# Optimization experiments

Hardware: AMD Instinct MI355X
Metric: run time of the kernel (lower is better)

## Reference

```python
import jax, jax.numpy as jnp
import numpy as np

B, C, H, W = 4, 384, 64, 64
NH = 8
HD = C // NH
SR = 2
SCALE = HD ** -0.5
Hs, Ws = H // SR, W // SR
NK = Hs * Ws


def setup_inputs() -> dict:
    key = jax.random.key(0)
    ks = jax.random.split(key, 8)
    s = 0.02
    return {
        "x": jax.random.normal(ks[0], (B, C, H, W), jnp.float32),
        "Wq": jax.random.normal(ks[1], (C, C), jnp.float32) * s,
        "Wk": jax.random.normal(ks[2], (C, C), jnp.float32) * s,
        "Wv": jax.random.normal(ks[3], (C, C), jnp.float32) * s,
        "Wsr": jax.random.normal(ks[4], (C, C, SR, SR), jnp.float32) * s,
        "bsr": jnp.zeros((C,), jnp.float32),
        "Wp": jax.random.normal(ks[5], (C, C), jnp.float32) * s,
        "bp": jnp.zeros((C,), jnp.float32),
        "rel_h": jax.random.normal(ks[6], (1, NH, HD, 1, Hs), jnp.float32),
        "rel_w": jax.random.normal(ks[7], (1, NH, HD, Ws, 1), jnp.float32),
    }


def _mhsa(x, Wq, Wk, Wv, Wsr, bsr, Wp, bp, rel_h, rel_w):
    Bq = x.shape[0]
    # 1x1 conv == channel matmul
    q = jnp.einsum('oc,bchw->bohw', Wq, x).reshape(Bq, NH, HD, H * W)
    # spatial reduction: Conv2d(kernel=SR, stride=SR); norm defaults to Identity
    xsr = jax.lax.conv_general_dilated(
        x, Wsr, window_strides=(SR, SR), padding='VALID',
        dimension_numbers=('NCHW', 'OIHW', 'NCHW')) + bsr[None, :, None, None]
    k = jnp.einsum('oc,bchw->bohw', Wk, xsr).reshape(Bq, NH, HD, NK)
    v = jnp.einsum('oc,bchw->bohw', Wv, xsr).reshape(Bq, NH, HD, NK)
    # relative positional bias fused into keys
    pos = (rel_h + rel_w).reshape(1, NH, HD, NK)
    k = (k + pos) * SCALE
    # attn[b,h,n,m] = q^T k, softmax over keys (dropout is identity at p=0)
    attn = jax.nn.softmax(jnp.einsum('bhdn,bhdm->bhnm', q, k), axis=-1)
    out = jnp.einsum('bhdm,bhnm->bhdn', v, attn).reshape(Bq, C, H, W)
    out = jnp.einsum('oc,bchw->bohw', Wp, out) + bp[None, :, None, None]
    return out


def reference(x, Wq, Wk, Wv, Wsr, bsr, Wp, bp, rel_h, rel_w):
    return _mhsa(x, Wq, Wk, Wv, Wsr, bsr, Wp, bp, rel_h, rel_w)
```

## Files before the change

### kernel.cpp

```cpp
#include <hip/hip_runtime.h>
#include <hip/hip_bf16.h>
#include <math.h>

typedef __attribute__((ext_vector_type(8))) short b16x8;
typedef __attribute__((ext_vector_type(4))) short b16x4;
typedef __attribute__((ext_vector_type(4))) float floatx4;
typedef __attribute__((ext_vector_type(16))) float f32x16;

constexpr int BATCH = 4, CCH = 384, NQ = 4096, NHD = 8, HDIM = 48, NK = 1024;
constexpr float SCALE = 0.14433756729740643f;
constexpr float SCALE_L2E = 0.14433756729740643f * 1.4426950408889634f;

__device__ inline unsigned short f2bf(float f) {
    unsigned u = __builtin_bit_cast(unsigned, f);
    u += 0x7fffu + ((u >> 16) & 1u);
    return (unsigned short)(u >> 16);
}

__device__ __forceinline__ void g2lds16(const void* g, void* l) {
    __builtin_amdgcn_global_load_lds(
        (const __attribute__((address_space(1))) unsigned int*)g,
        (__attribute__((address_space(3))) unsigned int*)l, 16, 0, 0);
}

__global__ void cvt_all(const float* __restrict__ Wq, const float* __restrict__ Wk,
                        const float* __restrict__ Wv, const float* __restrict__ Wsr,
                        const float* __restrict__ Wp,
                        short* __restrict__ WqB, short* __restrict__ WkvB,
                        short* __restrict__ WsrB, short* __restrict__ WpB) {
    int job = blockIdx.y;
    if (job == 3) {
        for (int i = blockIdx.x * 256 + threadIdx.x; i < 589824; i += gridDim.x * 256) {
            int o = i / 1536, r = i - o * 1536;
            WsrB[o * 1536 + (r & 3) * 384 + (r >> 2)] = (short)f2bf(Wsr[i]);
        }
        return;
    }
    const float* src; short* dst;
    if (job == 0)      { src = Wq;  dst = WqB; }
    else if (job == 1) { src = Wk;  dst = WkvB; }
    else if (job == 2) { src = Wv;  dst = WkvB + 147456; }
    else               { src = Wp;  dst = WpB; }
    for (int i = blockIdx.x * 256 + threadIdx.x; i < 147456; i += gridDim.x * 256)
        dst[i] = (short)f2bf(src[i]);
}

__global__ void t1_kern(const float* __restrict__ x, short* __restrict__ xT) {
    int b = blockIdx.z, s = blockIdx.x * 64 + (threadIdx.x & 63);
    for (int c8 = blockIdx.y * 8 + (threadIdx.x >> 6); c8 < blockIdx.y * 8 + 8; c8 += 4) {
        b16x8 pk;
        #pragma unroll
        for (int e = 0; e < 8; e++)
            pk[e] = (short)f2bf(x[((size_t)b * CCH + c8 * 8 + e) * NQ + s]);
        *(b16x8*)(xT + ((size_t)b * NQ + s) * CCH + c8 * 8) = pk;
    }
}

__global__ __launch_bounds__(256, 2) void fused_gemm1(
    const short* __restrict__ WsrB, const short* __restrict__ WqB,
    const short* __restrict__ xT, const float* __restrict__ bsr,
    short* __restrict__ xsrT, short* __restrict__ qTb)
{
    __shared__ short At[128 * 64];
    __shared__ short Bt[128 * 64];
    const int b = blockIdx.z;
    const int id = blockIdx.x;
    const bool conv = id < 24;
    const int sx = conv ? (id & 7) : ((id - 24) & 31);
    const int oy = conv ? (id >> 3) : ((id - 24) >> 5);
    const int Ks = conv ? 1536 : 384;
    const int S  = conv ? NK : NQ;
    const short* A = conv ? WsrB : WqB;
    short* Yt = conv ? xsrT : qTb;
    const int o0 = oy * 128, s0 = sx * 128;
    const int t = threadIdx.x, wave = t >> 6, lane = t & 63, g = lane >> 4, li = lane & 15;
    const int wr = wave >> 1, wc = wave & 1;
    floatx4 acc[4][4] = {};
    const short* Bbase = xT + (size_t)b * NQ * CCH;

    for (int k0 = 0; k0 < Ks; k0 += 64) {
        __syncthreads();
        #pragma unroll
        for (int it = 0; it < 4; it++) {
            int task = it * 256 + t;
            int row = task >> 3, ch = task & 7;
            int cont = ch ^ (row & 7);
            g2lds16(A + (size_t)(o0 + row) * Ks + k0 + cont * 8, At + task * 8);
        }
        #pragma unroll
        for (int it = 0; it < 4; it++) {
            int task = it * 256 + t;
            int row = task >> 3, ch = task & 7;
            int cont = ch ^ (row & 7);
            if (conv) {
                int ssr = s0 + row;
                int hs = ssr >> 5, wsv = ssr & 31;
                int k = k0 + cont * 8;
                int p = k / 384, coff = k - p * 384;
                g2lds16(Bbase + (size_t)((2 * hs + (p >> 1)) * 64 + 2 * wsv + (p & 1)) * 384 + coff,
                        Bt + task * 8);
            } else {
                g2lds16(Bbase + (size_t)(s0 + row) * 384 + k0 + cont * 8, Bt + task * 8);
            }
        }
        __syncthreads();
        #pragma unroll
        for (int kk = 0; kk < 2; kk++) {
            b16x8 af[4], bf[4];
            #pragma unroll
            for (int mi = 0; mi < 4; mi++) {
                int r = wr * 64 + mi * 16 + li;
                af[mi] = *(const b16x8*)(At + r * 64 + (((kk * 4 + g) ^ (r & 7)) * 8));
            }
            #pragma unroll
            for (int nf = 0; nf < 4; nf++) {
                int r = wc * 64 + nf * 16 + li;
                bf[nf] = *(const b16x8*)(Bt + r * 64 + (((kk * 4 + g) ^ (r & 7)) * 8));
            }
            #pragma unroll
            for (int mi = 0; mi < 4; mi++)
                #pragma unroll
                for (int nf = 0; nf < 4; nf++)
                    acc[mi][nf] = __builtin_amdgcn_mfma_f32_16x16x32_bf16(af[mi], bf[nf], acc[mi][nf], 0, 0, 0);
        }
    }

    #pragma unroll
    for (int mi = 0; mi < 4; mi++) {
        #pragma unroll
        for (int nf = 0; nf < 4; nf++) {
            int o = o0 + wr * 64 + mi * 16 + g * 4;
            int s = s0 + wc * 64 + nf * 16 + li;
            b16x4 pk;
            #pragma unroll
            for (int j = 0; j < 4; j++) {
                float v = acc[mi][nf][j];
                if (conv) v += bsr[o + j];
                pk[j] = (short)f2bf(v);
            }
            *(b16x4*)(Yt + ((size_t)b * S + s) * CCH + o) = pk;
        }
    }
}

template<int EPI>
__global__ __launch_bounds__(256, 2) void mfma_gemm(
    const short* __restrict__ A, const short* __restrict__ Bm,
    short* __restrict__ Yt, short* __restrict__ Y2, float* __restrict__ Yf,
    const float* __restrict__ bias, const float* __restrict__ relh,
    const float* __restrict__ relw, int Ksz, int S)
{
    __shared__ short At[128 * 64];
    __shared__ short Bt[128 * 64];
    const int b = blockIdx.z, o0 = blockIdx.y * 128, s0 = blockIdx.x * 128;
    const int t = threadIdx.x, wave = t >> 6, lane = t & 63, g = lane >> 4, li = lane & 15;
    const int wr = wave >> 1, wc = wave & 1;
    floatx4 acc[4][4] = {};
    const short* Bbase = Bm + (size_t)b * S * Ksz;

    for (int k0 = 0; k0 < Ksz; k0 += 64) {
        __syncthreads();
        #pragma unroll
        for (int it = 0; it < 4; it++) {
            int task = it * 256 + t;
            int row = task >> 3, ch = task & 7;
            int cont = ch ^ (row & 7);
            g2lds16(A + (size_t)(o0 + row) * Ksz + k0 + cont * 8, At + task * 8);
        }
        #pragma unroll
        for (int it = 0; it < 4; it++) {
            int task = it * 256 + t;
            int row = task >> 3, ch = task & 7;
            int cont = ch ^ (row & 7);
            g2lds16(Bbase + (size_t)(s0 + row) * Ksz + k0 + cont * 8, Bt + task * 8);
        }
        __syncthreads();
        #pragma unroll
        for (int kk = 0; kk < 2; kk++) {
            b16x8 af[4], bf[4];
            #pragma unroll
            for (int mi = 0; mi < 4; mi++) {
                int r = wr * 64 + mi * 16 + li;
                af[mi] = *(const b16x8*)(At + r * 64 + (((kk * 4 + g) ^ (r & 7)) * 8));
            }
            #pragma unroll
            for (int nf = 0; nf < 4; nf++) {
                int r = wc * 64 + nf * 16 + li;
                bf[nf] = *(const b16x8*)(Bt + r * 64 + (((kk * 4 + g) ^ (r & 7)) * 8));
            }
            #pragma unroll
            for (int mi = 0; mi < 4; mi++)
                #pragma unroll
                for (int nf = 0; nf < 4; nf++)
                    acc[mi][nf] = __builtin_amdgcn_mfma_f32_16x16x32_bf16(af[mi], bf[nf], acc[mi][nf], 0, 0, 0);
        }
    }

    #pragma unroll
    for (int mi = 0; mi < 4; mi++) {
        #pragma unroll
        for (int nf = 0; nf < 4; nf++) {
            int o = o0 + wr * 64 + mi * 16 + g * 4;
            int s = s0 + wc * 64 + nf * 16 + li;
            if constexpr (EPI == 2) {
                if (o0 < 384) {
                    int hs = s >> 5, wsv = s & 31;
                    b16x4 pk;
                    #pragma unroll
                    for (int j = 0; j < 4; j++)
                        pk[j] = (short)f2bf((acc[mi][nf][j] + relh[(o + j) * 32 + wsv]
                                             + relw[(o + j) * 32 + hs]) * SCALE_L2E);
                    *(b16x4*)(Yt + ((size_t)b * S + s) * CCH + o) = pk;
                } else {
                    #pragma unroll
                    for (int j = 0; j < 4; j++)
                        Y2[((size_t)b * CCH + (o - 384 + j)) * NK + s] = (short)f2bf(acc[mi][nf][j]);
                }
            } else {
                #pragma unroll
                for (int j = 0; j < 4; j++)
                    Yf[((size_t)b * CCH + o + j) * (size_t)S + s] = acc[mi][nf][j] + bias[o + j];
            }
        }
    }
}

__global__ __launch_bounds__(256, 4) void attn_kern(
    const short* __restrict__ qT, const short* __restrict__ kT,
    const short* __restrict__ vC, short* __restrict__ attT)
{
    __shared__ short Kl[2][6 * 64 * 8];
    __shared__ short Vl[2][8 * 64 * 8];
    const int wgid = blockIdx.x;
    const int nid = (wgid & 7) * 128 + (wgid >> 3);
    const int qt = nid & 31, hh = (nid >> 5) & 7, b = nid >> 8;
    const int t = threadIdx.x, wave = t >> 6, lane = t & 63;
    const int h = lane >> 5, c = lane & 31;
    const int n0 = qt * 128 + wave * 32;

    const short* qp = qT + (size_t)b * NQ * CCH + hh * HDIM;
    const short* kp = kT + (size_t)b * NK * CCH + hh * HDIM;
    const short* vp = vC + ((size_t)b * CCH + hh * HDIM) * NK;

    {
        int bufi = t >> 7, rem = t & 127;
        int ch = rem >> 4, row = 48 + (rem & 15);
        b16x8 val = {};
        if (row == 48)
            #pragma unroll
            for (int e = 0; e < 8; e++) val[e] = (short)0x3F80;
        *(b16x8*)(&Vl[bufi][(ch * 64 + row) * 8]) = val;
    }

    b16x8 qf[3];
    #pragma unroll
    for (int dc = 0; dc < 3; dc++)
        qf[dc] = *(const b16x8*)(qp + (size_t)(n0 + c) * CCH + dc * 16 + h * 8);

    auto stage = [&](int m0, int bi) {
        #pragma unroll
        for (int it = 0; it < 2; it++) {
            int task = it * 256 + wave * 64 + lane;
            int ch = task >> 6, row = task & 63;
            if (ch < 6) {
                int key = (row & 51) | ((row & 4) << 1) | ((row & 8) >> 1);
                g2lds16(kp + (size_t)(m0 + key) * CCH + ch * 8, &Kl[bi][task * 8]);
            }
        }
        #pragma unroll
        for (int it = 0; it < 2; it++) {
            int task = it * 256 + wave * 64 + lane;
            int ch = task >> 6, row = task & 63;
            if (row < 48)
                g2lds16(vp + (size_t)row * NK + m0 + ch * 8, &Vl[bi][task * 8]);
        }
    };

    f32x16 O[2] = {};

    stage(0, 0);
    for (int tt = 0; tt < 16; ++tt) {
        __syncthreads();
        if (tt < 15) stage((tt + 1) * 64, (tt + 1) & 1);
        const short* Kb = Kl[tt & 1];
        const short* Vb = Vl[tt & 1];
        #pragma unroll
        for (int kb = 0; kb < 2; kb++) {
            b16x8 kf[3];
            #pragma unroll
            for (int dc = 0; dc < 3; dc++)
                kf[dc] = *(const b16x8*)(Kb + (((dc * 2 + h) * 64) + kb * 32 + c) * 8);
            f32x16 s = {};
            __builtin_amdgcn_s_setprio(1);
            #pragma unroll
            for (int dc = 0; dc < 3; dc++)
                s = __builtin_amdgcn_mfma_f32_32x32x16_bf16(kf[dc], qf[dc], s, 0, 0, 0);
            __builtin_amdgcn_s_setprio(0);
            float p[16];
            #pragma unroll
            for (int r = 0; r < 16; r++) p[r] = exp2f(s[r]);
            b16x8 pfrag[2];
            #pragma unroll
            for (int kk = 0; kk < 2; kk++) {
                union { unsigned u[4]; b16x8 v; } w;
                #pragma unroll
                for (int wd = 0; wd < 4; wd++)
                    asm("v_cvt_pk_bf16_f32 %0, %1, %2"
                        : "=v"(w.u[wd])
                        : "v"(p[kk * 8 + wd * 2]), "v"(p[kk * 8 + wd * 2 + 1]));
                pfrag[kk] = w.v;
            }
            __builtin_amdgcn_s_setprio(1);
            #pragma unroll
            for (int kk = 0; kk < 2; kk++)
                #pragma unroll
                for (int db = 0; db < 2; db++) {
                    b16x8 vf = *(const b16x8*)(Vb + (((kb * 4 + kk * 2 + h) * 64) + db * 32 + c) * 8);
                    O[db] = __builtin_amdgcn_mfma_f32_32x32x16_bf16(pfrag[kk], vf, O[db], 0, 0, 0);
                }
            __builtin_amdgcn_s_setprio(0);
        }
    }

    __syncthreads();
    short* Olw = ((short*)Vl) + wave * 2048;
    #pragma unroll
    for (int r = 0; r < 16; r++) {
        int qrow = (r & 3) + 8 * (r >> 2) + 4 * h;
        float lr = __shfl(O[1][r], (lane & 32) | 16);
        float iq = 1.0f / lr;
        #pragma unroll
        for (int db = 0; db < 2; db++) {
            int d = db * 32 + c;
            if (d < 48)
                Olw[qrow * 64 + (((d >> 3) ^ (qrow & 7)) * 8) + (d & 7)] =
                    (short)f2bf(O[db][r] * iq);
        }
    }
    __syncthreads();
    #pragma unroll
    for (int it = 0; it < 4; it++) {
        int idx = it * 64 + lane;
        int row = idx >> 3, c8 = idx & 7;
        if (c8 < 6) {
            b16x8 val = *(const b16x8*)(Olw + row * 64 + ((c8 ^ (row & 7)) * 8));
            *(b16x8*)(attT + ((size_t)b * NQ + n0 + row) * CCH + hh * HDIM + c8 * 8) = val;
        }
    }
}

extern "C" void kernel_launch(void* const* d_in, const int* in_sizes, int n_in,
                              void* d_out, int out_size, void* d_ws, size_t ws_size,
                              hipStream_t stream) {
    const float* x    = (const float*)d_in[0];
    const float* Wq   = (const float*)d_in[1];
    const float* Wk   = (const float*)d_in[2];
    const float* Wv   = (const float*)d_in[3];
    const float* Wsr  = (const float*)d_in[4];
    const float* bsr  = (const float*)d_in[5];
    const float* Wp   = (const float*)d_in[6];
    const float* bp   = (const float*)d_in[7];
    const float* relh = (const float*)d_in[8];
    const float* relw = (const float*)d_in[9];
    float* out = (float*)d_out;

    short* ws = (short*)d_ws;
    size_t off = 0;
    auto alloc = [&](size_t n) { short* p = ws + off; off += n; return p; };
    short* WqB  = alloc(147456);
    short* WkvB = alloc(294912);
    short* WsrB = alloc(589824);
    short* WpB  = alloc(147456);
    short* xT   = alloc((size_t)BATCH * NQ * CCH);
    short* xsrT = alloc((size_t)BATCH * NK * CCH);
    short* qTb  = alloc((size_t)BATCH * NQ * CCH);
    short* kTb  = alloc((size_t)BATCH * NK * CCH);
    short* vCb  = alloc((size_t)BATCH * CCH * NK);
    short* attT = alloc((size_t)BATCH * NQ * CCH);

    cvt_all<<<dim3(576, 5), 256, 0, stream>>>(Wq, Wk, Wv, Wsr, Wp, WqB, WkvB, WsrB, WpB);
    t1_kern<<<dim3(64, 6, BATCH), 256, 0, stream>>>(x, xT);
    fused_gemm1<<<dim3(120, 1, BATCH), 256, 0, stream>>>(WsrB, WqB, xT, bsr, xsrT, qTb);
    mfma_gemm<2><<<dim3(8, 6, BATCH), 256, 0, stream>>>(
        WkvB, xsrT, kTb, vCb, nullptr, nullptr, relh, relw, 384, NK);
    attn_kern<<<dim3(1024), 256, 0, stream>>>(qTb, kTb, vCb, attT);
    mfma_gemm<3><<<dim3(32, 3, BATCH), 256, 0, stream>>>(
        WpB, attT, nullptr, nullptr, out, bp, nullptr, nullptr, 384, NQ);
}
```

Baseline: 128.0 us.

## Fold spatial-reduction conv into K/V weights to remove intermediate GEMM

Precomputes combined weights Wc = [Wk;Wv]·Wsr (plus a folded bias kvb = W·bsr) once per call, so K and V come straight from x in one 1536-deep GEMM fused with the Q projection. This drops the separate xsr intermediate and one kernel launch with its write and read round trip. The trade is more FLOPs, since 768×1536 replaces 384×1536 plus 768×384 on 1024 columns per batch. It also adds a weight-combine GEMM, a precomputation kernel, and an extra bf16 rounding of the combined weights. Separately, softmax exp switches to the hardware exp2 builtin.

```diff
diff --git a/kernel.cpp b/kernel.cpp
--- a/kernel.cpp
+++ b/kernel.cpp
@@ -25,14 +25,27 @@
 
 __global__ void cvt_all(const float* __restrict__ Wq, const float* __restrict__ Wk,
                         const float* __restrict__ Wv, const float* __restrict__ Wsr,
-                        const float* __restrict__ Wp,
+                        const float* __restrict__ Wp, const float* __restrict__ bsr,
                         short* __restrict__ WqB, short* __restrict__ WkvB,
-                        short* __restrict__ WsrB, short* __restrict__ WpB) {
+                        short* __restrict__ WsrT, short* __restrict__ WpB,
+                        float* __restrict__ kvb) {
     int job = blockIdx.y;
     if (job == 3) {
-        for (int i = blockIdx.x * 256 + threadIdx.x; i < 589824; i += gridDim.x * 256) {
-            int o = i / 1536, r = i - o * 1536;
-            WsrB[o * 1536 + (r & 3) * 384 + (r >> 2)] = (short)f2bf(Wsr[i]);
+        for (int j = blockIdx.x * 256 + threadIdx.x; j < 589824; j += gridDim.x * 256) {
+            int kin = j / 384, o = j - kin * 384;
+            int p = kin / 384, cin = kin - p * 384;
+            WsrT[j] = (short)f2bf(Wsr[o * 1536 + cin * 4 + p]);
+        }
+        return;
+    }
+    if (job == 5) {
+        int o2 = blockIdx.x * 256 + threadIdx.x;
+        if (o2 < 768) {
+            const float* wrow = (o2 < 384) ? (Wk + (size_t)o2 * 384)
+                                           : (Wv + (size_t)(o2 - 384) * 384);
+            float ssum = 0.f;
+            for (int c = 0; c < 384; c++) ssum += wrow[c] * bsr[c];
+            kvb[o2] = ssum;
         }
         return;
     }
@@ -56,22 +69,84 @@
     }
 }
 
-__global__ __launch_bounds__(256, 2) void fused_gemm1(
-    const short* __restrict__ WsrB, const short* __restrict__ WqB,
-    const short* __restrict__ xT, const float* __restrict__ bsr,
-    short* __restrict__ xsrT, short* __restrict__ qTb)
+__global__ __launch_bounds__(256, 2) void combine_gemm(
+    const short* __restrict__ WsrT, const short* __restrict__ WkvB,
+    short* __restrict__ Wc)
+{
+    __shared__ short At[128 * 64];
+    __shared__ short Bt[128 * 64];
+    const int o0 = blockIdx.y * 128, s0 = blockIdx.x * 128;
+    const int t = threadIdx.x, wave = t >> 6, lane = t & 63, g = lane >> 4, li = lane & 15;
+    const int wr = wave >> 1, wc = wave & 1;
+    floatx4 acc[4][4] = {};
+
+    for (int k0 = 0; k0 < 384; k0 += 64) {
+        __syncthreads();
+        #pragma unroll
+        for (int it = 0; it < 4; it++) {
+            int task = it * 256 + t;
+            int row = task >> 3, ch = task & 7;
+            int cont = ch ^ (row & 7);
+            g2lds16(WsrT + (size_t)(o0 + row) * 384 + k0 + cont * 8, At + task * 8);
+        }
+        #pragma unroll
+        for (int it = 0; it < 4; it++) {
+            int task = it * 256 + t;
+            int row = task >> 3, ch = task & 7;
+            int cont = ch ^ (row & 7);
+            g2lds16(WkvB + (size_t)(s0 + row) * 384 + k0 + cont * 8, Bt + task * 8);
+        }
+        __syncthreads();
+        #pragma unroll
+        for (int kk = 0; kk < 2; kk++) {
+            b16x8 af[4], bf[4];
+            #pragma unroll
+            for (int mi = 0; mi < 4; mi++) {
+                int r = wr * 64 + mi * 16 + li;
+                af[mi] = *(const b16x8*)(At + r * 64 + (((kk * 4 + g) ^ (r & 7)) * 8));
+            }
+            #pragma unroll
+            for (int nf = 0; nf < 4; nf++) {
+                int r = wc * 64 + nf * 16 + li;
+                bf[nf] = *(const b16x8*)(Bt + r * 64 + (((kk * 4 + g) ^ (r & 7)) * 8));
+            }
+            #pragma unroll
+            for (int mi = 0; mi < 4; mi++)
+                #pragma unroll
+                for (int nf = 0; nf < 4; nf++)
+                    acc[mi][nf] = __builtin_amdgcn_mfma_f32_16x16x32_bf16(af[mi], bf[nf], acc[mi][nf], 0, 0, 0);
+        }
+    }
+
+    #pragma unroll
+    for (int mi = 0; mi < 4; mi++) {
+        #pragma unroll
+        for (int nf = 0; nf < 4; nf++) {
+            int o = o0 + wr * 64 + mi * 16 + g * 4;
+            int s = s0 + wc * 64 + nf * 16 + li;
+            b16x4 pk;
+            #pragma unroll
+            for (int j = 0; j < 4; j++) pk[j] = (short)f2bf(acc[mi][nf][j]);
+            *(b16x4*)(Wc + (size_t)s * 1536 + o) = pk;
+        }
+    }
+}
+
+__global__ __launch_bounds__(256, 2) void fused_qkv(
+    const short* __restrict__ WqB, const short* __restrict__ Wc,
+    const short* __restrict__ xT, const float* __restrict__ kvb,
+    const float* __restrict__ relh, const float* __restrict__ relw,
+    short* __restrict__ qTb, short* __restrict__ kTb, short* __restrict__ vCb)
 {
     __shared__ short At[128 * 64];
     __shared__ short Bt[128 * 64];
     const int b = blockIdx.z;
     const int id = blockIdx.x;
-    const bool conv = id < 24;
-    const int sx = conv ? (id & 7) : ((id - 24) & 31);
-    const int oy = conv ? (id >> 3) : ((id - 24) >> 5);
-    const int Ks = conv ? 1536 : 384;
-    const int S  = conv ? NK : NQ;
-    const short* A = conv ? WsrB : WqB;
-    short* Yt = conv ? xsrT : qTb;
+    const bool kv = id >= 96;
+    const int sx = kv ? ((id - 96) & 7) : (id & 31);
+    const int oy = kv ? ((id - 96) >> 3) : (id >> 5);
+    const int Ks = kv ? 1536 : 384;
+    const short* A = kv ? Wc : WqB;
     const int o0 = oy * 128, s0 = sx * 128;
     const int t = threadIdx.x, wave = t >> 6, lane = t & 63, g = lane >> 4, li = lane & 15;
     const int wr = wave >> 1, wc = wave & 1;
@@ -92,7 +167,7 @@
             int task = it * 256 + t;
             int row = task >> 3, ch = task & 7;
             int cont = ch ^ (row & 7);
-            if (conv) {
+            if (kv) {
                 int ssr = s0 + row;
                 int hs = ssr >> 5, wsv = ssr & 31;
                 int k = k0 + cont * 8;
@@ -131,24 +206,33 @@
         for (int nf = 0; nf < 4; nf++) {
             int o = o0 + wr * 64 + mi * 16 + g * 4;
             int s = s0 + wc * 64 + nf * 16 + li;
-            b16x4 pk;
-            #pragma unroll
-            for (int j = 0; j < 4; j++) {
-                float v = acc[mi][nf][j];
-                if (conv) v += bsr[o + j];
-                pk[j] = (short)f2bf(v);
-            }
-            *(b16x4*)(Yt + ((size_t)b * S + s) * CCH + o) = pk;
-        }
-    }
-}
-
-template<int EPI>
-__global__ __launch_bounds__(256, 2) void mfma_gemm(
+            if (!kv) {
+                b16x4 pk;
+                #pragma unroll
+                for (int j = 0; j < 4; j++) pk[j] = (short)f2bf(acc[mi][nf][j]);
+                *(b16x4*)(qTb + ((size_t)b * NQ + s) * CCH + o) = pk;
+            } else if (o0 < 384) {
+                int hs = s >> 5, wsv = s & 31;
+                b16x4 pk;
+                #pragma unroll
+                for (int j = 0; j < 4; j++)
+                    pk[j] = (short)f2bf((acc[mi][nf][j] + kvb[o + j]
+                                         + relh[(o + j) * 32 + wsv]
+                                         + relw[(o + j) * 32 + hs]) * SCALE_L2E);
+                *(b16x4*)(kTb + ((size_t)b * NK + s) * CCH + o) = pk;
+            } else {
+                #pragma unroll
+                for (int j = 0; j < 4; j++)
+                    vCb[((size_t)b * CCH + (o - 384 + j)) * NK + s] =
+                        (short)f2bf(acc[mi][nf][j] + kvb[o + j]);
+            }
+        }
+    }
+}
+
+__global__ __launch_bounds__(256, 2) void p_gemm(
     const short* __restrict__ A, const short* __restrict__ Bm,
-    short* __restrict__ Yt, short* __restrict__ Y2, float* __restrict__ Yf,
-    const float* __restrict__ bias, const float* __restrict__ relh,
-    const float* __restrict__ relw, int Ksz, int S)
+    float* __restrict__ Yf, const float* __restrict__ bias)
 {
     __shared__ short At[128 * 64];
     __shared__ short Bt[128 * 64];
@@ -156,23 +240,23 @@
     const int t = threadIdx.x, wave = t >> 6, lane = t & 63, g = lane >> 4, li = lane & 15;
     const int wr = wave >> 1, wc = wave & 1;
     floatx4 acc[4][4] = {};
-    const short* Bbase = Bm + (size_t)b * S * Ksz;
-
-    for (int k0 = 0; k0 < Ksz; k0 += 64) {
-        __syncthreads();
-        #pragma unroll
-        for (int it = 0; it < 4; it++) {
-            int task = it * 256 + t;
-            int row = task >> 3, ch = task & 7;
-            int cont = ch ^ (row & 7);
-            g2lds16(A + (size_t)(o0 + row) * Ksz + k0 + cont * 8, At + task * 8);
-        }
-        #pragma unroll
-        for (int it = 0; it < 4; it++) {
-            int task = it * 256 + t;
-            int row = task >> 3, ch = task & 7;
-            int cont = ch ^ (row & 7);
-            g2lds16(Bbase + (size_t)(s0 + row) * Ksz + k0 + cont * 8, Bt + task * 8);
+    const short* Bbase = Bm + (size_t)b * NQ * CCH;
+
+    for (int k0 = 0; k0 < 384; k0 += 64) {
+        __syncthreads();
+        #pragma unroll
+        for (int it = 0; it < 4; it++) {
+            int task = it * 256 + t;
+            int row = task >> 3, ch = task & 7;
+            int cont = ch ^ (row & 7);
+            g2lds16(A + (size_t)(o0 + row) * 384 + k0 + cont * 8, At + task * 8);
+        }
+        #pragma unroll
+        for (int it = 0; it < 4; it++) {
+            int task = it * 256 + t;
+            int row = task >> 3, ch = task & 7;
+            int cont = ch ^ (row & 7);
+            g2lds16(Bbase + (size_t)(s0 + row) * 384 + k0 + cont * 8, Bt + task * 8);
         }
         __syncthreads();
         #pragma unroll
@@ -202,25 +286,9 @@
         for (int nf = 0; nf < 4; nf++) {
             int o = o0 + wr * 64 + mi * 16 + g * 4;
             int s = s0 + wc * 64 + nf * 16 + li;
-            if constexpr (EPI == 2) {
-                if (o0 < 384) {
-                    int hs = s >> 5, wsv = s & 31;
-                    b16x4 pk;
-                    #pragma unroll
-                    for (int j = 0; j < 4; j++)
-                        pk[j] = (short)f2bf((acc[mi][nf][j] + relh[(o + j) * 32 + wsv]
-                                             + relw[(o + j) * 32 + hs]) * SCALE_L2E);
-                    *(b16x4*)(Yt + ((size_t)b * S + s) * CCH + o) = pk;
-                } else {
-                    #pragma unroll
-                    for (int j = 0; j < 4; j++)
-                        Y2[((size_t)b * CCH + (o - 384 + j)) * NK + s] = (short)f2bf(acc[mi][nf][j]);
-                }
-            } else {
-                #pragma unroll
-                for (int j = 0; j < 4; j++)
-                    Yf[((size_t)b * CCH + o + j) * (size_t)S + s] = acc[mi][nf][j] + bias[o + j];
-            }
+            #pragma unroll
+            for (int j = 0; j < 4; j++)
+                Yf[((size_t)b * CCH + o + j) * (size_t)NQ + s] = acc[mi][nf][j] + bias[o + j];
         }
     }
 }
@@ -298,7 +366,8 @@
             __builtin_amdgcn_s_setprio(0);
             float p[16];
             #pragma unroll
-            for (int r = 0; r < 16; r++) p[r] = exp2f(s[r]);
+            for (int r = 0; r < 16; r++)
+                p[r] = __builtin_amdgcn_exp2f(s[r]);
             b16x8 pfrag[2];
             #pragma unroll
             for (int kk = 0; kk < 2; kk++) {
@@ -369,21 +438,23 @@
     auto alloc = [&](size_t n) { short* p = ws + off; off += n; return p; };
     short* WqB  = alloc(147456);
     short* WkvB = alloc(294912);
-    short* WsrB = alloc(589824);
+    short* WsrT = alloc(589824);
     short* WpB  = alloc(147456);
+    short* WcB  = alloc(768 * 1536);
+    short* kvbh = alloc(768 * 2);
     short* xT   = alloc((size_t)BATCH * NQ * CCH);
-    short* xsrT = alloc((size_t)BATCH * NK * CCH);
     short* qTb  = alloc((size_t)BATCH * NQ * CCH);
     short* kTb  = alloc((size_t)BATCH * NK * CCH);
     short* vCb  = alloc((size_t)BATCH * CCH * NK);
     short* attT = alloc((size_t)BATCH * NQ * CCH);
-
-    cvt_all<<<dim3(576, 5), 256, 0, stream>>>(Wq, Wk, Wv, Wsr, Wp, WqB, WkvB, WsrB, WpB);
+    float* kvb  = (float*)kvbh;
+
+    cvt_all<<<dim3(576, 6), 256, 0, stream>>>(Wq, Wk, Wv, Wsr, Wp, bsr,
+                                              WqB, WkvB, WsrT, WpB, kvb);
+    combine_gemm<<<dim3(6, 12), 256, 0, stream>>>(WsrT, WkvB, WcB);
     t1_kern<<<dim3(64, 6, BATCH), 256, 0, stream>>>(x, xT);
-    fused_gemm1<<<dim3(120, 1, BATCH), 256, 0, stream>>>(WsrB, WqB, xT, bsr, xsrT, qTb);
-    mfma_gemm<2><<<dim3(8, 6, BATCH), 256, 0, stream>>>(
-        WkvB, xsrT, kTb, vCb, nullptr, nullptr, relh, relw, 384, NK);
+    fused_qkv<<<dim3(144, 1, BATCH), 256, 0, stream>>>(
+        WqB, WcB, xT, kvb, relh, relw, qTb, kTb, vCb);
     attn_kern<<<dim3(1024), 256, 0, stream>>>(qTb, kTb, vCb, attT);
-    mfma_gemm<3><<<dim3(32, 3, BATCH), 256, 0, stream>>>(
-        WpB, attT, nullptr, nullptr, out, bp, nullptr, nullptr, 384, NQ);
-}
+    p_gemm<<<dim3(32, 3, BATCH), 256, 0, stream>>>(WpB, attT, out, bp);
+}
```

Measured after the change: 126.1 us. Within noise of the previous version (-1.5%).
